# Kernel tuning notes

Measured on AMD Instinct MI355X. Metric: run time of the kernel, lower is better.

## Reference

```python
import jax, jax.numpy as jnp
import numpy as np


def setup_inputs() -> dict:
    key = jax.random.key(0)
    k1, k2, k3, k4 = jax.random.split(key, 4)
    B, Nq, Nk, D = 8, 2048, 2048, 768
    return {
        "query": jax.random.normal(k1, (B, Nq, D), dtype=jnp.float32),
        "key": jax.random.normal(k2, (Nk, D), dtype=jnp.float32),
        "x": jax.random.normal(k3, (B, Nk, D), dtype=jnp.float32),
        "W": jax.random.normal(k4, (D, D), dtype=jnp.float32) * (1.0 / np.sqrt(D)),
        "b": jnp.zeros((D,), dtype=jnp.float32),
    }


def reference(query, key, x, W, b):
    # Linear projection: [B,Nq,dk] @ W^T + b -> [B,Nq,dq]
    query_proj = jnp.einsum("bqd,ed->bqe", query, W) + b
    # tensordot over dim_query: [B,Nq,dq] x [Nk,dq] -> [B,Nq,Nk]
    score = jnp.einsum("bqe,ke->bqk", query_proj, key)
    attn = jax.nn.softmax(score, axis=-1)
    # bmm: [B,Nq,Nk] @ [B,Nk,Dv] -> [B,Nq,Dv]
    out = jnp.einsum("bqk,bkd->bqd", attn, x)
    return (out, attn)
```

## Files before the change

kernel.cpp:

```cpp
#include <hip/hip_runtime.h>

typedef short s16x8 __attribute__((ext_vector_type(8)));
typedef _Float16 h16x8 __attribute__((ext_vector_type(8)));
typedef float f32x4 __attribute__((ext_vector_type(4)));

__device__ __forceinline__ unsigned short f2bf(float f) {
    unsigned int u = __builtin_bit_cast(unsigned int, f);
    u += 0x7FFFu + ((u >> 16) & 1u);
    return (unsigned short)(u >> 16);
}
__device__ __forceinline__ float bf2f(unsigned short h) {
    unsigned int u = ((unsigned int)h) << 16;
    return __builtin_bit_cast(float, u);
}
__device__ __forceinline__ unsigned short f2h(float f) {
    _Float16 h = (_Float16)f;
    return __builtin_bit_cast(unsigned short, h);
}
__device__ __forceinline__ float h2f(unsigned short u) {
    return (float)__builtin_bit_cast(_Float16, u);
}

__device__ __forceinline__ int swz(int row, int kbyte) {
    return (row * 64 + kbyte) ^ (((row >> 1) & 3) << 4);
}

__device__ __forceinline__ void gl16(const void* g, void* l) {
    __builtin_amdgcn_global_load_lds(
        (__attribute__((address_space(1))) void*)(g),
        (__attribute__((address_space(3))) void*)(l), 16, 0, 0);
}


__global__ __launch_bounds__(256, 1) void score_2ph(
    const unsigned short* __restrict__ A, const unsigned short* __restrict__ Bm,
    const float* __restrict__ bias, float* __restrict__ C,
    int M, int N, int K, int nbx)
{
    __shared__ unsigned short lds[2][2][128 * 64];

    const int bid = blockIdx.x;
    const int cpx = gridDim.x >> 3;
    const int sw  = (bid & 7) * cpx + (bid >> 3);
    const int m0 = (sw / nbx) * 128, n0 = (sw % nbx) * 128;

    const int t = threadIdx.x;
    const int l = t & 63, w = t >> 6;
    const int rm = (w >> 1) * 64, cn = (w & 1) * 64;
    const int lr = l & 15;
    const int kg16 = (l >> 4) * 16;

    const int jrow   = l >> 3;
    const int srcoff = ((l & 7) ^ jrow) << 3;

    const unsigned short* gA = A  + (long)(m0 + jrow) * K + srcoff;
    const unsigned short* gB = Bm + (long)(n0 + jrow) * K + srcoff;

    f32x4 acc[4][4];
    #pragma unroll
    for (int i = 0; i < 4; ++i)
        #pragma unroll
        for (int j = 0; j < 4; ++j)
            acc[i][j] = (f32x4){0.f, 0.f, 0.f, 0.f};

    const int nt = K >> 6;
    #pragma unroll
    for (int i = 0; i < 4; ++i) {
        const int c = w * 4 + i;
        gl16(gA + (long)(8 * c) * K, &lds[0][0][c * 512]);
        gl16(gB + (long)(8 * c) * K, &lds[0][1][c * 512]);
    }
    __syncthreads();

    int p = 0;
    for (int it = 0; it < nt; ++it) {
        if (it + 1 < nt) {
            const unsigned short* nA = gA + (it + 1) * 64;
            const unsigned short* nB = gB + (it + 1) * 64;
            #pragma unroll
            for (int i = 0; i < 4; ++i) {
                const int c = w * 4 + i;
                gl16(nA + (long)(8 * c) * K, &lds[p ^ 1][0][c * 512]);
                gl16(nB + (long)(8 * c) * K, &lds[p ^ 1][1][c * 512]);
            }
        }
        const char* baseA = (const char*)&lds[p][0][0];
        const char* baseB = (const char*)&lds[p][1][0];
        h16x8 af[2][4], bf[2][4];
        #pragma unroll
        for (int ks = 0; ks < 2; ++ks)
            #pragma unroll
            for (int mi = 0; mi < 4; ++mi) {
                const int row = rm + mi * 16 + lr;
                af[ks][mi] = *(const h16x8*)(baseA + row * 128 +
                                ((ks * 64 + kg16) ^ ((row & 7) << 4)));
            }
        #pragma unroll
        for (int ks = 0; ks < 2; ++ks)
            #pragma unroll
            for (int nj = 0; nj < 4; ++nj) {
                const int row = cn + nj * 16 + lr;
                bf[ks][nj] = *(const h16x8*)(baseB + row * 128 +
                                ((ks * 64 + kg16) ^ ((row & 7) << 4)));
            }
        #pragma unroll
        for (int ks = 0; ks < 2; ++ks)
            #pragma unroll
            for (int mi = 0; mi < 4; ++mi)
                #pragma unroll
                for (int nj = 0; nj < 4; ++nj)
                    acc[mi][nj] = __builtin_amdgcn_mfma_f32_16x16x32_f16(
                        af[ks][mi], bf[ks][nj], acc[mi][nj], 0, 0, 0);
        __syncthreads();
        p ^= 1;
    }

    #pragma unroll
    for (int mi = 0; mi < 4; ++mi) {
        #pragma unroll
        for (int nj = 0; nj < 4; ++nj) {
            const int row = m0 + rm + mi * 16 + (l >> 4) * 4;
            const int col = n0 + cn + nj * 16 + lr;
            const float badd = bias[col];
            #pragma unroll
            for (int r = 0; r < 4; ++r)
                C[(long)(row + r) * N + col] = acc[mi][nj][r] + badd;
        }
    }
}

__global__ __launch_bounds__(256, 1) void pv_2ph(
    const unsigned short* __restrict__ A, const unsigned short* __restrict__ Bm,
    float* __restrict__ C, int M, int N, int K,
    long strideA, long strideB, long strideC)
{
    __shared__ unsigned short lds[2][2][128 * 64];

    const int bz = blockIdx.z;
    const unsigned short* Ab = A  + (long)bz * strideA;
    const unsigned short* Bb = Bm + (long)bz * strideB;
    float* Cb = C + (long)bz * strideC;
    const int m0 = blockIdx.x * 128, n0 = blockIdx.y * 128;

    const int t = threadIdx.x;
    const int l = t & 63, w = t >> 6;
    const int rm = (w >> 1) * 64, cn = (w & 1) * 64;
    const int lr = l & 15;
    const int kg16 = (l >> 4) * 16;

    const int jrow   = l >> 3;
    const int srcoff = ((l & 7) ^ jrow) << 3;

    const unsigned short* gA = Ab + (long)(m0 + jrow) * K + srcoff;
    const unsigned short* gB = Bb + (long)(n0 + jrow) * K + srcoff;

    f32x4 acc[4][4];
    #pragma unroll
    for (int i = 0; i < 4; ++i)
        #pragma unroll
        for (int j = 0; j < 4; ++j)
            acc[i][j] = (f32x4){0.f, 0.f, 0.f, 0.f};

    const int nt = K >> 6;
    #pragma unroll
    for (int i = 0; i < 4; ++i) {
        const int c = w * 4 + i;
        gl16(gA + (long)(8 * c) * K, &lds[0][0][c * 512]);
        gl16(gB + (long)(8 * c) * K, &lds[0][1][c * 512]);
    }
    __syncthreads();

    int p = 0;
    for (int it = 0; it < nt; ++it) {
        if (it + 1 < nt) {
            const unsigned short* nA = gA + (it + 1) * 64;
            const unsigned short* nB = gB + (it + 1) * 64;
            #pragma unroll
            for (int i = 0; i < 4; ++i) {
                const int c = w * 4 + i;
                gl16(nA + (long)(8 * c) * K, &lds[p ^ 1][0][c * 512]);
                gl16(nB + (long)(8 * c) * K, &lds[p ^ 1][1][c * 512]);
            }
        }
        const char* baseA = (const char*)&lds[p][0][0];
        const char* baseB = (const char*)&lds[p][1][0];
        h16x8 af[2][4], bf[2][4];
        #pragma unroll
        for (int ks = 0; ks < 2; ++ks)
            #pragma unroll
            for (int mi = 0; mi < 4; ++mi) {
                const int row = rm + mi * 16 + lr;
                af[ks][mi] = *(const h16x8*)(baseA + row * 128 +
                                ((ks * 64 + kg16) ^ ((row & 7) << 4)));
            }
        #pragma unroll
        for (int ks = 0; ks < 2; ++ks)
            #pragma unroll
            for (int nj = 0; nj < 4; ++nj) {
                const int row = cn + nj * 16 + lr;
                bf[ks][nj] = *(const h16x8*)(baseB + row * 128 +
                                ((ks * 64 + kg16) ^ ((row & 7) << 4)));
            }
        #pragma unroll
        for (int ks = 0; ks < 2; ++ks)
            #pragma unroll
            for (int mi = 0; mi < 4; ++mi)
                #pragma unroll
                for (int nj = 0; nj < 4; ++nj)
                    acc[mi][nj] = __builtin_amdgcn_mfma_f32_16x16x32_f16(
                        af[ks][mi], bf[ks][nj], acc[mi][nj], 0, 0, 0);
        __syncthreads();
        p ^= 1;
    }

    #pragma unroll
    for (int mi = 0; mi < 4; ++mi) {
        #pragma unroll
        for (int nj = 0; nj < 4; ++nj) {
            const int row = m0 + rm + mi * 16 + (l >> 4) * 4;
            const int col = n0 + cn + nj * 16 + lr;
            #pragma unroll
            for (int r = 0; r < 4; ++r)
                Cb[(long)(row + r) * N + col] = acc[mi][nj][r];
        }
    }
}

template<int SPLIT, bool TRANSB, bool BIAS>
__global__ __launch_bounds__(256, 1) void mfma_gemm(
    const float* __restrict__ A, const float* __restrict__ Bsrc,
    const float* __restrict__ bias, float* __restrict__ C,
    int M, int N, int K, long strideA, long strideB, long strideC)
{
    constexpr int NB = (SPLIT > 1) ? 2 : 1;
    __shared__ unsigned short sA[NB][128 * 32];
    __shared__ unsigned short sB[NB][128 * 32];

    const int t  = threadIdx.x;
    const int bz = blockIdx.z;
    const float* Ab = A    + (long)bz * strideA;
    const float* Bb = Bsrc + (long)bz * strideB;
    float*       Cb = C    + (long)bz * strideC;
    const int m0 = blockIdx.y * 128;
    const int n0 = blockIdx.x * 128;

    const int l  = t & 63, w = t >> 6;
    const int rm = (w >> 1) * 64;
    const int cn = (w & 1) * 64;
    const int lr = l & 15;
    const int kg = (l >> 4) * 16;

    const int srow = t >> 1;
    const int skh  = (t & 1) * 16;
    const int s_ = t & 15;
    const int kp = t >> 4;

    f32x4 acc[4][4];
    #pragma unroll
    for (int i = 0; i < 4; ++i)
        #pragma unroll
        for (int j = 0; j < 4; ++j)
            acc[i][j] = (f32x4){0.f, 0.f, 0.f, 0.f};

    for (int kt = 0; kt < K; kt += 32) {
        {
            const float* p = &Ab[(long)(m0 + srow) * K + kt + skh];
            float f[16];
            #pragma unroll
            for (int q = 0; q < 4; ++q) {
                const float4 v = *(const float4*)(p + 4 * q);
                f[4*q+0] = v.x; f[4*q+1] = v.y; f[4*q+2] = v.z; f[4*q+3] = v.w;
            }
            s16x8 h0, h1, l0, l1;
            #pragma unroll
            for (int q = 0; q < 8; ++q) {
                unsigned short h = f2bf(f[q]);      h0[q] = (short)h;
                if (SPLIT > 1) l0[q] = (short)f2bf(f[q] - bf2f(h));
                unsigned short g = f2bf(f[8 + q]);  h1[q] = (short)g;
                if (SPLIT > 1) l1[q] = (short)f2bf(f[8 + q] - bf2f(g));
            }
            *(s16x8*)((char*)sA[0] + swz(srow, skh * 2))      = h0;
            *(s16x8*)((char*)sA[0] + swz(srow, skh * 2 + 16)) = h1;
            if (SPLIT > 1) {
                *(s16x8*)((char*)sA[1] + swz(srow, skh * 2))      = l0;
                *(s16x8*)((char*)sA[1] + swz(srow, skh * 2 + 16)) = l1;
            }
        }
        if (!TRANSB) {
            const float* p = &Bb[(long)(n0 + srow) * K + kt + skh];
            float f[16];
            #pragma unroll
            for (int q = 0; q < 4; ++q) {
                const float4 v = *(const float4*)(p + 4 * q);
                f[4*q+0] = v.x; f[4*q+1] = v.y; f[4*q+2] = v.z; f[4*q+3] = v.w;
            }
            s16x8 h0, h1, l0, l1;
            #pragma unroll
            for (int q = 0; q < 8; ++q) {
                unsigned short h = f2bf(f[q]);      h0[q] = (short)h;
                if (SPLIT > 1) l0[q] = (short)f2bf(f[q] - bf2f(h));
                unsigned short g = f2bf(f[8 + q]);  h1[q] = (short)g;
                if (SPLIT > 1) l1[q] = (short)f2bf(f[8 + q] - bf2f(g));
            }
            *(s16x8*)((char*)sB[0] + swz(srow, skh * 2))      = h0;
            *(s16x8*)((char*)sB[0] + swz(srow, skh * 2 + 16)) = h1;
            if (SPLIT > 1) {
                *(s16x8*)((char*)sB[1] + swz(srow, skh * 2))      = l0;
                *(s16x8*)((char*)sB[1] + swz(srow, skh * 2 + 16)) = l1;
            }
        } else {
            const float* r0 = &Bb[(long)(kt + 2 * kp) * N + n0 + s_ * 8];
            const float* r1 = r0 + N;
            float a0[8], a1[8];
            {
                const float4 u0 = *(const float4*)(r0);
                const float4 u1 = *(const float4*)(r0 + 4);
                const float4 v0 = *(const float4*)(r1);
                const float4 v1 = *(const float4*)(r1 + 4);
                a0[0]=u0.x;a0[1]=u0.y;a0[2]=u0.z;a0[3]=u0.w;
                a0[4]=u1.x;a0[5]=u1.y;a0[6]=u1.z;a0[7]=u1.w;
                a1[0]=v0.x;a1[1]=v0.y;a1[2]=v0.z;a1[3]=v0.w;
                a1[4]=v1.x;a1[5]=v1.y;a1[6]=v1.z;a1[7]=v1.w;
            }
            #pragma unroll
            for (int j = 0; j < 8; ++j) {
                const int i  = (j + s_) & 7;
                const int nl = s_ * 8 + i;
                const unsigned int val =
                    (unsigned int)f2bf(a0[i]) | ((unsigned int)f2bf(a1[i]) << 16);
                *(unsigned int*)((char*)sB[0] + swz(nl, 4 * kp)) = val;
            }
        }
        __syncthreads();

        s16x8 ah[4], bh[4];
        #pragma unroll
        for (int mi = 0; mi < 4; ++mi)
            ah[mi] = *(const s16x8*)((const char*)sA[0] + swz(rm + mi * 16 + lr, kg));
        #pragma unroll
        for (int nj = 0; nj < 4; ++nj)
            bh[nj] = *(const s16x8*)((const char*)sB[0] + swz(cn + nj * 16 + lr, kg));
        #pragma unroll
        for (int mi = 0; mi < 4; ++mi)
            #pragma unroll
            for (int nj = 0; nj < 4; ++nj)
                acc[mi][nj] = __builtin_amdgcn_mfma_f32_16x16x32_bf16(
                    ah[mi], bh[nj], acc[mi][nj], 0, 0, 0);
        if (SPLIT > 1) {
            s16x8 al[4], bl[4];
            #pragma unroll
            for (int mi = 0; mi < 4; ++mi)
                al[mi] = *(const s16x8*)((const char*)sA[1] + swz(rm + mi * 16 + lr, kg));
            #pragma unroll
            for (int mi = 0; mi < 4; ++mi)
                #pragma unroll
                for (int nj = 0; nj < 4; ++nj)
                    acc[mi][nj] = __builtin_amdgcn_mfma_f32_16x16x32_bf16(
                        al[mi], bh[nj], acc[mi][nj], 0, 0, 0);
            #pragma unroll
            for (int nj = 0; nj < 4; ++nj)
                bl[nj] = *(const s16x8*)((const char*)sB[1] + swz(cn + nj * 16 + lr, kg));
            #pragma unroll
            for (int mi = 0; mi < 4; ++mi)
                #pragma unroll
                for (int nj = 0; nj < 4; ++nj)
                    acc[mi][nj] = __builtin_amdgcn_mfma_f32_16x16x32_bf16(
                        ah[mi], bl[nj], acc[mi][nj], 0, 0, 0);
        }
        __syncthreads();
    }

    #pragma unroll
    for (int mi = 0; mi < 4; ++mi) {
        #pragma unroll
        for (int nj = 0; nj < 4; ++nj) {
            const int row = m0 + rm + mi * 16 + (l >> 4) * 4;
            const int col = n0 + cn + nj * 16 + lr;
            const float badd = BIAS ? bias[col] : 0.f;
            #pragma unroll
            for (int r = 0; r < 4; ++r)
                Cb[(long)(row + r) * N + col] = acc[mi][nj][r] + badd;
        }
    }
}

__global__ __launch_bounds__(256, 1) void score_gemm(
    const unsigned short* __restrict__ Ah, const unsigned short* __restrict__ Al,
    const unsigned short* __restrict__ Bh, const unsigned short* __restrict__ Bl,
    const float* __restrict__ bias, float* __restrict__ C,
    int M, int N, int K, int nbx)
{
    __shared__ unsigned short sAh[128 * 32];
    __shared__ unsigned short sBh[128 * 32];
    __shared__ unsigned short sAl[128 * 32];
    __shared__ unsigned short sBl[128 * 32];

    const int bid = blockIdx.x;
    const int cpx = gridDim.x >> 3;
    const int sw  = (bid & 7) * cpx + (bid >> 3);
    const int mb  = sw / nbx, nb = sw % nbx;
    const int m0 = mb * 128, n0 = nb * 128;

    const int t = threadIdx.x;
    const int l = t & 63, w = t >> 6;
    const int rm = (w >> 1) * 64;
    const int cn = (w & 1) * 64;
    const int lr = l & 15;
    const int kg = (l >> 4) * 16;

    const int r0 = 2 * w, r1 = 2 * w + 1;
    const int rowS0 = 16 * r0 + (l >> 2);
    const int rowS1 = 16 * r1 + (l >> 2);
    const int h0 = (l & 3) ^ ((rowS0 >> 1) & 3);
    const int h1 = (l & 3) ^ ((rowS1 >> 1) & 3);

    const unsigned short* gAh0 = Ah + (long)(m0 + rowS0) * K + 8 * h0;
    const unsigned short* gAh1 = Ah + (long)(m0 + rowS1) * K + 8 * h1;
    const unsigned short* gAl0 = Al + (long)(m0 + rowS0) * K + 8 * h0;
    const unsigned short* gAl1 = Al + (long)(m0 + rowS1) * K + 8 * h1;
    const unsigned short* gBh0 = Bh + (long)(n0 + rowS0) * K + 8 * h0;
    const unsigned short* gBh1 = Bh + (long)(n0 + rowS1) * K + 8 * h1;
    const unsigned short* gBl0 = Bl + (long)(n0 + rowS0) * K + 8 * h0;
    const unsigned short* gBl1 = Bl + (long)(n0 + rowS1) * K + 8 * h1;

    unsigned short* dA0 = &sAh[r0 * 512];
    unsigned short* dA1 = &sAh[r1 * 512];
    unsigned short* dAl0 = &sAl[r0 * 512];
    unsigned short* dAl1 = &sAl[r1 * 512];
    unsigned short* dB0 = &sBh[r0 * 512];
    unsigned short* dB1 = &sBh[r1 * 512];
    unsigned short* dBl0 = &sBl[r0 * 512];
    unsigned short* dBl1 = &sBl[r1 * 512];

    f32x4 acc[4][4];
    #pragma unroll
    for (int i = 0; i < 4; ++i)
        #pragma unroll
        for (int j = 0; j < 4; ++j)
            acc[i][j] = (f32x4){0.f, 0.f, 0.f, 0.f};

    const int nk = K >> 5;
    for (int it = 0; it < nk; ++it) {
        gl16(gAh0, dA0);  gl16(gAh1, dA1);
        gl16(gBh0, dB0);  gl16(gBh1, dB1);
        gl16(gAl0, dAl0); gl16(gAl1, dAl1);
        gl16(gBl0, dBl0); gl16(gBl1, dBl1);
        gAh0 += 32; gAh1 += 32; gAl0 += 32; gAl1 += 32;
        gBh0 += 32; gBh1 += 32; gBl0 += 32; gBl1 += 32;
        __syncthreads();

        s16x8 ah[4], bh[4];
        #pragma unroll
        for (int mi = 0; mi < 4; ++mi)
            ah[mi] = *(const s16x8*)((const char*)sAh + swz(rm + mi * 16 + lr, kg));
        #pragma unroll
        for (int nj = 0; nj < 4; ++nj)
            bh[nj] = *(const s16x8*)((const char*)sBh + swz(cn + nj * 16 + lr, kg));
        #pragma unroll
        for (int mi = 0; mi < 4; ++mi)
            #pragma unroll
            for (int nj = 0; nj < 4; ++nj)
                acc[mi][nj] = __builtin_amdgcn_mfma_f32_16x16x32_bf16(
                    ah[mi], bh[nj], acc[mi][nj], 0, 0, 0);
        s16x8 al[4], bl[4];
        #pragma unroll
        for (int mi = 0; mi < 4; ++mi)
            al[mi] = *(const s16x8*)((const char*)sAl + swz(rm + mi * 16 + lr, kg));
        #pragma unroll
        for (int mi = 0; mi < 4; ++mi)
            #pragma unroll
            for (int nj = 0; nj < 4; ++nj)
                acc[mi][nj] = __builtin_amdgcn_mfma_f32_16x16x32_bf16(
                    al[mi], bh[nj], acc[mi][nj], 0, 0, 0);
        #pragma unroll
        for (int nj = 0; nj < 4; ++nj)
            bl[nj] = *(const s16x8*)((const char*)sBl + swz(cn + nj * 16 + lr, kg));
        #pragma unroll
        for (int mi = 0; mi < 4; ++mi)
            #pragma unroll
            for (int nj = 0; nj < 4; ++nj)
                acc[mi][nj] = __builtin_amdgcn_mfma_f32_16x16x32_bf16(
                    ah[mi], bl[nj], acc[mi][nj], 0, 0, 0);
        __syncthreads();
    }

    #pragma unroll
    for (int mi = 0; mi < 4; ++mi) {
        #pragma unroll
        for (int nj = 0; nj < 4; ++nj) {
            const int row = m0 + rm + mi * 16 + (l >> 4) * 4;
            const int col = n0 + cn + nj * 16 + lr;
            const float badd = bias[col];
            #pragma unroll
            for (int r = 0; r < 4; ++r)
                C[(long)(row + r) * N + col] = acc[mi][nj][r] + badd;
        }
    }
}

__global__ __launch_bounds__(256, 1) void out_gemm(
    const float* __restrict__ A32, const unsigned short* __restrict__ B16,
    float* __restrict__ C, int M, int N, int K,
    long strideA, long strideB, long strideC)
{
    __shared__ unsigned short sA[128 * 32];
    __shared__ unsigned short sB[128 * 32];

    const int bz = blockIdx.z;
    const float* Ab = A32 + (long)bz * strideA;
    const unsigned short* Bb = B16 + (long)bz * strideB;
    float* Cb = C + (long)bz * strideC;
    const int m0 = blockIdx.x * 128;
    const int n0 = blockIdx.y * 128;

    const int t = threadIdx.x;
    const int l = t & 63, w = t >> 6;
    const int rm = (w >> 1) * 64;
    const int cn = (w & 1) * 64;
    const int lr = l & 15;
    const int kg = (l >> 4) * 16;

    const int r0 = 2 * w, r1 = 2 * w + 1;
    const int rowS0 = 16 * r0 + (l >> 2);
    const int rowS1 = 16 * r1 + (l >> 2);
    const int h0 = (l & 3) ^ ((rowS0 >> 1) & 3);
    const int h1 = (l & 3) ^ ((rowS1 >> 1) & 3);
    const unsigned short* gB0 = Bb + (long)(n0 + rowS0) * K + 8 * h0;
    const unsigned short* gB1 = Bb + (long)(n0 + rowS1) * K + 8 * h1;
    unsigned short* dB0 = &sB[r0 * 512];
    unsigned short* dB1 = &sB[r1 * 512];

    const int srow = t >> 1;
    const int skh  = (t & 1) * 16;
    const float* gA = &Ab[(long)(m0 + srow) * K + skh];

    f32x4 acc[4][4];
    #pragma unroll
    for (int i = 0; i < 4; ++i)
        #pragma unroll
        for (int j = 0; j < 4; ++j)
            acc[i][j] = (f32x4){0.f, 0.f, 0.f, 0.f};

    const int nk = K >> 5;
    for (int it = 0; it < nk; ++it) {
        gl16(gB0, dB0); gl16(gB1, dB1);
        gB0 += 32; gB1 += 32;
        {
            float f[16];
            #pragma unroll
            for (int q = 0; q < 4; ++q) {
                const float4 v = *(const float4*)(gA + 4 * q);
                f[4*q+0] = v.x; f[4*q+1] = v.y; f[4*q+2] = v.z; f[4*q+3] = v.w;
            }
            gA += 32;
            s16x8 v0, v1;
            #pragma unroll
            for (int q = 0; q < 8; ++q) {
                v0[q] = (short)f2bf(f[q]);
                v1[q] = (short)f2bf(f[8 + q]);
            }
            *(s16x8*)((char*)sA + swz(srow, skh * 2))      = v0;
            *(s16x8*)((char*)sA + swz(srow, skh * 2 + 16)) = v1;
        }
        __syncthreads();

        s16x8 ah[4], bh[4];
        #pragma unroll
        for (int mi = 0; mi < 4; ++mi)
            ah[mi] = *(const s16x8*)((const char*)sA + swz(rm + mi * 16 + lr, kg));
        #pragma unroll
        for (int nj = 0; nj < 4; ++nj)
            bh[nj] = *(const s16x8*)((const char*)sB + swz(cn + nj * 16 + lr, kg));
        #pragma unroll
        for (int mi = 0; mi < 4; ++mi)
            #pragma unroll
            for (int nj = 0; nj < 4; ++nj)
                acc[mi][nj] = __builtin_amdgcn_mfma_f32_16x16x32_bf16(
                    ah[mi], bh[nj], acc[mi][nj], 0, 0, 0);
        __syncthreads();
    }

    #pragma unroll
    for (int mi = 0; mi < 4; ++mi) {
        #pragma unroll
        for (int nj = 0; nj < 4; ++nj) {
            const int row = m0 + rm + mi * 16 + (l >> 4) * 4;
            const int col = n0 + cn + nj * 16 + lr;
            #pragma unroll
            for (int r = 0; r < 4; ++r)
                Cb[(long)(row + r) * N + col] = acc[mi][nj][r];
        }
    }
}

template<int MODE>
__global__ __launch_bounds__(256) void transpose64(
    const float* __restrict__ in, void* __restrict__ outv,
    int R, int Cc, long sIn, long sOut)
{
    __shared__ float tl[64][65];
    const int z = blockIdx.z;
    const float* ib = in + (long)z * sIn;
    const int r0 = blockIdx.x * 64, c0 = blockIdx.y * 64;
    const int t = threadIdx.x;
    const int lrr = t >> 4, lc = (t & 15) * 4;
    #pragma unroll
    for (int p = 0; p < 4; ++p) {
        const float4 v = *(const float4*)&ib[(long)(r0 + lrr + 16 * p) * Cc + c0 + lc];
        tl[lrr + 16 * p][lc + 0] = v.x; tl[lrr + 16 * p][lc + 1] = v.y;
        tl[lrr + 16 * p][lc + 2] = v.z; tl[lrr + 16 * p][lc + 3] = v.w;
    }
    __syncthreads();
    #pragma unroll
    for (int p = 0; p < 4; ++p) {
        const int orow = c0 + lrr + 16 * p;
        const int ocol = r0 + lc;
        const float a = tl[lc + 0][lrr + 16 * p];
        const float b = tl[lc + 1][lrr + 16 * p];
        const float c = tl[lc + 2][lrr + 16 * p];
        const float d = tl[lc + 3][lrr + 16 * p];
        if (MODE == 1) {
            ushort4 u = { f2bf(a), f2bf(b), f2bf(c), f2bf(d) };
            *(ushort4*)((unsigned short*)outv + (long)z * sOut + (long)orow * R + ocol) = u;
        } else if (MODE == 2) {
            ushort4 u = { f2h(a), f2h(b), f2h(c), f2h(d) };
            *(ushort4*)((unsigned short*)outv + (long)z * sOut + (long)orow * R + ocol) = u;
        } else {
            float4 u = { a, b, c, d };
            *(float4*)((float*)outv + (long)z * sOut + (long)orow * R + ocol) = u;
        }
    }
}

__global__ __launch_bounds__(256) void convert_hilo(
    const float* __restrict__ src, unsigned short* __restrict__ hi,
    unsigned short* __restrict__ lo, long n8)
{
    for (long i = (long)blockIdx.x * blockDim.x + threadIdx.x; i < n8;
         i += (long)gridDim.x * blockDim.x) {
        const float4 a = *(const float4*)&src[i * 8];
        const float4 b = *(const float4*)&src[i * 8 + 4];
        const float f[8] = { a.x, a.y, a.z, a.w, b.x, b.y, b.z, b.w };
        s16x8 h, lv;
        #pragma unroll
        for (int q = 0; q < 8; ++q) {
            const unsigned short hh = f2bf(f[q]);
            h[q]  = (short)hh;
            lv[q] = (short)f2bf(f[q] - bf2f(hh));
        }
        *(s16x8*)&hi[i * 8] = h;
        *(s16x8*)&lo[i * 8] = lv;
    }
}

__global__ __launch_bounds__(256) void convert_q_ilv(
    const float* __restrict__ src, unsigned short* __restrict__ dst,
    int kd8, long n8)
{
    const int Kd = kd8 * 8;
    for (long i = (long)blockIdx.x * blockDim.x + threadIdx.x; i < n8;
         i += (long)gridDim.x * blockDim.x) {
        const long row = i / kd8;
        const int  col = (int)(i - row * kd8) * 8;
        const float4 a = *(const float4*)&src[i * 8];
        const float4 b = *(const float4*)&src[i * 8 + 4];
        const float f[8] = { a.x, a.y, a.z, a.w, b.x, b.y, b.z, b.w };
        s16x8 h, lv;
        #pragma unroll
        for (int q = 0; q < 8; ++q) {
            const unsigned short hh = f2h(f[q]);
            h[q]  = (short)hh;
            lv[q] = (short)f2h(f[q] - h2f(hh));
        }
        unsigned short* dr = dst + row * (long)(2 * Kd);
        *(s16x8*)&dr[col]      = h;
        *(s16x8*)&dr[Kd + col] = lv;
    }
}

__global__ __launch_bounds__(256) void convert_kw_dup(
    const float* __restrict__ src, unsigned short* __restrict__ dst,
    int kd8, long n8)
{
    const int Kd = kd8 * 8;
    for (long i = (long)blockIdx.x * blockDim.x + threadIdx.x; i < n8;
         i += (long)gridDim.x * blockDim.x) {
        const long row = i / kd8;
        const int  col = (int)(i - row * kd8) * 8;
        const float4 a = *(const float4*)&src[i * 8];
        const float4 b = *(const float4*)&src[i * 8 + 4];
        const float f[8] = { a.x, a.y, a.z, a.w, b.x, b.y, b.z, b.w };
        s16x8 h;
        #pragma unroll
        for (int q = 0; q < 8; ++q) h[q] = (short)f2h(f[q]);
        unsigned short* dr = dst + row * (long)(2 * Kd);
        *(s16x8*)&dr[col]      = h;
        *(s16x8*)&dr[Kd + col] = h;
    }
}

__global__ __launch_bounds__(256) void bk_dot(
    const float* __restrict__ key, const float* __restrict__ b,
    float* __restrict__ bk, int D)
{
    const int row = blockIdx.x * 4 + (threadIdx.x >> 6);
    const int l = threadIdx.x & 63;
    const float* kr = key + (long)row * D;
    float s = 0.f;
    for (int e = l; e < D; e += 64) s += kr[e] * b[e];
    #pragma unroll
    for (int off = 32; off > 0; off >>= 1) s += __shfl_xor(s, off);
    if (l == 0) bk[row] = s;
}

__global__ __launch_bounds__(256) void softmax_f16(
    float* __restrict__ S, unsigned short* __restrict__ S16, int cols)
{
    const long row = blockIdx.x;
    float* p = S + row * (long)cols;
    unsigned short* p16 = S16 + row * (long)cols;
    const int t = threadIdx.x;
    const int wid = t >> 6;
    const int base = t * 8;

    const float4 a = *(const float4*)&p[base];
    const float4 b = *(const float4*)&p[base + 4];
    float vals[8] = { a.x, a.y, a.z, a.w, b.x, b.y, b.z, b.w };
    float m = -INFINITY;
    #pragma unroll
    for (int i = 0; i < 8; ++i) m = fmaxf(m, vals[i]);
    #pragma unroll
    for (int off = 32; off > 0; off >>= 1)
        m = fmaxf(m, __shfl_xor(m, off));
    __shared__ float smax[4], ssum[4];
    if ((t & 63) == 0) smax[wid] = m;
    __syncthreads();
    m = fmaxf(fmaxf(smax[0], smax[1]), fmaxf(smax[2], smax[3]));

    float s = 0.f;
    #pragma unroll
    for (int i = 0; i < 8; ++i) {
        vals[i] = __expf(vals[i] - m);
        s += vals[i];
    }
    #pragma unroll
    for (int off = 32; off > 0; off >>= 1)
        s += __shfl_xor(s, off);
    if ((t & 63) == 0) ssum[wid] = s;
    __syncthreads();
    s = (ssum[0] + ssum[1]) + (ssum[2] + ssum[3]);
    const float inv = 1.0f / s;

    float4 o0, o1;
    o0.x = vals[0]*inv; o0.y = vals[1]*inv; o0.z = vals[2]*inv; o0.w = vals[3]*inv;
    o1.x = vals[4]*inv; o1.y = vals[5]*inv; o1.z = vals[6]*inv; o1.w = vals[7]*inv;
    *(float4*)&p[base]     = o0;
    *(float4*)&p[base + 4] = o1;
    s16x8 h;
    h[0]=(short)f2h(o0.x); h[1]=(short)f2h(o0.y); h[2]=(short)f2h(o0.z); h[3]=(short)f2h(o0.w);
    h[4]=(short)f2h(o1.x); h[5]=(short)f2h(o1.y); h[6]=(short)f2h(o1.z); h[7]=(short)f2h(o1.w);
    *(s16x8*)&p16[base] = h;
}

__global__ __launch_bounds__(256) void softmax_rows(float* __restrict__ S, int cols)
{
    const long row = blockIdx.x;
    float* p = S + row * (long)cols;
    const int t = threadIdx.x;
    const int wid = t >> 6;

    float vals[8];
    float m = -INFINITY;
    #pragma unroll
    for (int i = 0; i < 8; ++i) {
        vals[i] = p[t + i * 256];
        m = fmaxf(m, vals[i]);
    }
    #pragma unroll
    for (int off = 32; off > 0; off >>= 1)
        m = fmaxf(m, __shfl_xor(m, off));
    __shared__ float smax[4], ssum[4];
    if ((t & 63) == 0) smax[wid] = m;
    __syncthreads();
    m = fmaxf(fmaxf(smax[0], smax[1]), fmaxf(smax[2], smax[3]));

    float s = 0.f;
    #pragma unroll
    for (int i = 0; i < 8; ++i) {
        vals[i] = __expf(vals[i] - m);
        s += vals[i];
    }
    #pragma unroll
    for (int off = 32; off > 0; off >>= 1)
        s += __shfl_xor(s, off);
    if ((t & 63) == 0) ssum[wid] = s;
    __syncthreads();
    s = (ssum[0] + ssum[1]) + (ssum[2] + ssum[3]);
    const float inv = 1.0f / s;
    #pragma unroll
    for (int i = 0; i < 8; ++i)
        p[t + i * 256] = vals[i] * inv;
}

extern "C" void kernel_launch(void* const* d_in, const int* in_sizes, int n_in,
                              void* d_out, int out_size, void* d_ws, size_t ws_size,
                              hipStream_t stream)
{
    const float* query = (const float*)d_in[0];
    const float* key   = (const float*)d_in[1];
    const float* x     = (const float*)d_in[2];
    const float* W     = (const float*)d_in[3];
    const float* bias  = (const float*)d_in[4];

    const int D  = in_sizes[4];
    const int Nk = in_sizes[1] / D;
    const int B  = in_sizes[2] / (Nk * D);
    const int Nq = in_sizes[0] / (B * D);

    float* out  = (float*)d_out;
    float* attn = out + (long)B * Nq * D;

    const long nQ  = (long)B * Nq * D;
    const long nKW = (long)Nk * D;
    const long nX  = (long)B * Nk * D;
    const int  M   = B * Nq;
    const int  K2  = 2 * D;

    const size_t xTb    = (size_t)nX * 2;
    const size_t kwDupB = (size_t)Nk * K2 * 2;
    const size_t bkB    = (size_t)Nk * 4;
    const size_t atb1   = (size_t)Nq * Nk * 2;
    const size_t fixedB = xTb + kwDupB + bkB;
    const size_t qLob   = (size_t)nQ * 2;
    const size_t wsMid  = xTb + qLob;

    int g = 0;
    if (ws_size >= fixedB + 2 * atb1) {
        g = (int)((ws_size - fixedB) / atb1);
        if (g > B) g = B;
    }

    if (g >= 2) {
        unsigned short* qIlv  = (unsigned short*)out;
        unsigned short* xT     = (unsigned short*)d_ws;
        unsigned short* kwDup  = (unsigned short*)((char*)d_ws + xTb);
        float*          bk     = (float*)((char*)d_ws + xTb + kwDupB);
        unsigned short* attn16 = (unsigned short*)((char*)d_ws + fixedB);
        float* Wt  = attn;
        float* KWf = attn + 1048576;

        dim3 gtw(D / 64, D / 64, 1);
        transpose64<0><<<gtw, 256, 0, stream>>>(W, Wt, D, D, 0L, 0L);
        dim3 gkw(D / 128, Nk / 128, 1);
        mfma_gemm<3, false, false><<<gkw, 256, 0, stream>>>(
            key, Wt, nullptr, KWf, Nk, D, D, 0L, 0L, 0L);
        convert_kw_dup<<<768, 256, 0, stream>>>(KWf, kwDup, D / 8, nKW / 8);
        bk_dot<<<Nk / 4, 256, 0, stream>>>(key, bias, bk, D);
        convert_q_ilv<<<2048, 256, 0, stream>>>(query, qIlv, D / 8, nQ / 8);
        dim3 gtx(Nk / 64, D / 64, B);
        transpose64<2><<<gtx, 256, 0, stream>>>(
            x, xT, Nk, D, (long)Nk * D, (long)D * Nk);

        const int nbx = Nk / 128;
        const int nwg = (M / 128) * nbx;
        score_2ph<<<nwg, 256, 0, stream>>>(
            qIlv, kwDup, bk, attn, M, Nk, K2, nbx);

        for (int b0 = 0; b0 < B; b0 += g) {
            const int gb = (b0 + g <= B) ? g : (B - b0);
            softmax_f16<<<gb * Nq, 256, 0, stream>>>(
                attn + (long)b0 * Nq * Nk, attn16, Nk);
            dim3 go(Nq / 128, D / 128, gb);
            pv_2ph<<<go, 256, 0, stream>>>(
                attn16, xT + (long)b0 * D * Nk, out + (long)b0 * Nq * D,
                Nq, D, Nk, (long)Nq * Nk, (long)D * Nk, (long)Nq * D);
        }
    } else if (ws_size >= wsMid) {
        unsigned short* q_hi  = (unsigned short*)out;
        unsigned short* KW_hi = q_hi + nQ;
        unsigned short* KW_lo = KW_hi + nKW;
        float*          bk    = (float*)(KW_lo + nKW);
        unsigned short* q_lo  = (unsigned short*)d_ws;
        unsigned short* xT    = q_lo + nQ;
        float* Wt  = attn;
        float* KWf = attn + 1048576;

        dim3 gtw(D / 64, D / 64, 1);
        transpose64<0><<<gtw, 256, 0, stream>>>(W, Wt, D, D, 0L, 0L);
        dim3 gkw(D / 128, Nk / 128, 1);
        mfma_gemm<3, false, false><<<gkw, 256, 0, stream>>>(
            key, Wt, nullptr, KWf, Nk, D, D, 0L, 0L, 0L);
        convert_hilo<<<768, 256, 0, stream>>>(KWf, KW_hi, KW_lo, nKW / 8);
        bk_dot<<<Nk / 4, 256, 0, stream>>>(key, bias, bk, D);
        convert_hilo<<<2048, 256, 0, stream>>>(query, q_hi, q_lo, nQ / 8);
        dim3 gtx(Nk / 64, D / 64, B);
        transpose64<1><<<gtx, 256, 0, stream>>>(
            x, xT, Nk, D, (long)Nk * D, (long)D * Nk);
        const int nbx = Nk / 128;
        const int nwg = (B * Nq / 128) * nbx;
        score_gemm<<<nwg, 256, 0, stream>>>(
            q_hi, q_lo, KW_hi, KW_lo, bk, attn, B * Nq, Nk, D, nbx);
        softmax_rows<<<B * Nq, 256, 0, stream>>>(attn, Nk);
        dim3 go(Nq / 128, D / 128, B);
        out_gemm<<<go, 256, 0, stream>>>(
            attn, xT, out, Nq, D, Nk, (long)Nq * Nk, (long)D * Nk, (long)Nq * D);
    } else {
        float* qp = out;
        dim3 g1(D / 128, (B * Nq) / 128, 1);
        mfma_gemm<3, false, true><<<g1, 256, 0, stream>>>(
            query, W, bias, qp, B * Nq, D, D, 0L, 0L, 0L);
        dim3 g2(Nk / 128, Nq / 128, B);
        mfma_gemm<3, false, false><<<g2, 256, 0, stream>>>(
            qp, key, nullptr, attn, Nq, Nk, D, (long)Nq * D, 0L, (long)Nq * Nk);
        softmax_rows<<<B * Nq, 256, 0, stream>>>(attn, Nk);
        dim3 g4(D / 128, Nq / 128, B);
        mfma_gemm<1, true, false><<<g4, 256, 0, stream>>>(
            attn, x, nullptr, out, Nq, D, Nk, (long)Nq * Nk, (long)Nk * D, (long)Nq * D);
    }
}
```

Baseline: 347.9 us.

## Replace score GEMM with 256x256 tile, 8-wave, four-phase pipelined kernel

The score GEMM moves from a 128x128 tile with 4 waves and simple double buffering to a 256x256 tile with 8 waves. Each K-step is split into four sub-phases, with global-to-LDS loads for upcoming tiles interleaved between them using explicit vmcnt waits, barriers and raised priority around the MFMA bursts. The aim is more data reuse per tile and better overlap of memory traffic with MFMA compute. In exchange the block count drops fourfold, which may hurt occupancy and tail balance across CUs. The hand-tuned wait counts are also fragile.

```diff
diff --git a/kernel.cpp b/kernel.cpp
--- a/kernel.cpp
+++ b/kernel.cpp
@@ -31,102 +31,133 @@
         (__attribute__((address_space(3))) void*)(l), 16, 0, 0);
 }
 
-
-__global__ __launch_bounds__(256, 1) void score_2ph(
+#define STG(ptr, rowbase, tau, bufp, slot) do {                                     \
+    gl16((ptr) + (long)((rowbase) + sl) * K + (tau) * 64 + koff,                    \
+         &lds[bufp][slot][(unsigned)t * 8]);                                        \
+    gl16((ptr) + (long)((rowbase) + 64 + sl) * K + (tau) * 64 + koff,               \
+         &lds[bufp][slot][4096u + (unsigned)t * 8]);                                \
+} while (0)
+
+#define PH(bufp, qi, qj, VMSTR, STAGEBLOCK) do {                                    \
+    h16x8 af_[2][4], bf_[2][2];                                                     \
+    const char* baseA_ = (const char*)&lds[bufp][qi][0];                            \
+    const char* baseB_ = (const char*)&lds[bufp][2 + (qj)][0];                      \
+    _Pragma("unroll")                                                               \
+    for (int ks_ = 0; ks_ < 2; ++ks_) {                                             \
+        _Pragma("unroll")                                                           \
+        for (int f_ = 0; f_ < 4; ++f_) {                                            \
+            const int row_ = wm * 64 + f_ * 16 + lr;                                \
+            af_[ks_][f_] = *(const h16x8*)(baseA_ + row_ * 128 +                    \
+                            ((ks_ * 64 + kg16) ^ ((row_ & 7) << 4)));               \
+        }                                                                           \
+        _Pragma("unroll")                                                           \
+        for (int g_ = 0; g_ < 2; ++g_) {                                            \
+            const int row_ = wn * 32 + g_ * 16 + lr;                                \
+            bf_[ks_][g_] = *(const h16x8*)(baseB_ + row_ * 128 +                    \
+                            ((ks_ * 64 + kg16) ^ ((row_ & 7) << 4)));               \
+        }                                                                           \
+    }                                                                               \
+    STAGEBLOCK;                                                                     \
+    asm volatile("s_waitcnt vmcnt(" VMSTR ")" ::: "memory");                        \
+    __builtin_amdgcn_s_barrier();                                                   \
+    __builtin_amdgcn_sched_barrier(0);                                              \
+    __builtin_amdgcn_s_setprio(1);                                                  \
+    _Pragma("unroll")                                                               \
+    for (int ks_ = 0; ks_ < 2; ++ks_)                                               \
+        _Pragma("unroll")                                                           \
+        for (int f_ = 0; f_ < 4; ++f_)                                              \
+            _Pragma("unroll")                                                       \
+            for (int g_ = 0; g_ < 2; ++g_)                                          \
+                acc[qi][qj][f_][g_] = __builtin_amdgcn_mfma_f32_16x16x32_f16(       \
+                    af_[ks_][f_], bf_[ks_][g_], acc[qi][qj][f_][g_], 0, 0, 0);      \
+    __builtin_amdgcn_s_setprio(0);                                                  \
+    __builtin_amdgcn_s_barrier();                                                   \
+    __builtin_amdgcn_sched_barrier(0);                                              \
+} while (0)
+
+__global__ __launch_bounds__(512, 2) void score_8ph(
     const unsigned short* __restrict__ A, const unsigned short* __restrict__ Bm,
     const float* __restrict__ bias, float* __restrict__ C,
     int M, int N, int K, int nbx)
 {
-    __shared__ unsigned short lds[2][2][128 * 64];
+    __shared__ unsigned short lds[2][4][8192];
 
     const int bid = blockIdx.x;
     const int cpx = gridDim.x >> 3;
     const int sw  = (bid & 7) * cpx + (bid >> 3);
-    const int m0 = (sw / nbx) * 128, n0 = (sw % nbx) * 128;
+    const int m0 = (sw / nbx) * 256, n0 = (sw % nbx) * 256;
 
     const int t = threadIdx.x;
     const int l = t & 63, w = t >> 6;
-    const int rm = (w >> 1) * 64, cn = (w & 1) * 64;
+    const int wm = w >> 2, wn = w & 3;
     const int lr = l & 15;
     const int kg16 = (l >> 4) * 16;
 
-    const int jrow   = l >> 3;
-    const int srcoff = ((l & 7) ^ jrow) << 3;
-
-    const unsigned short* gA = A  + (long)(m0 + jrow) * K + srcoff;
-    const unsigned short* gB = Bm + (long)(n0 + jrow) * K + srcoff;
-
-    f32x4 acc[4][4];
-    #pragma unroll
-    for (int i = 0; i < 4; ++i)
-        #pragma unroll
-        for (int j = 0; j < 4; ++j)
-            acc[i][j] = (f32x4){0.f, 0.f, 0.f, 0.f};
+    const int sl   = w * 8 + (l >> 3);
+    const int koff = ((l & 7) ^ (sl & 7)) * 8;
+
+    f32x4 acc[2][2][4][2];
+    #pragma unroll
+    for (int a = 0; a < 2; ++a)
+        #pragma unroll
+        for (int b = 0; b < 2; ++b)
+            #pragma unroll
+            for (int c = 0; c < 4; ++c)
+                #pragma unroll
+                for (int d = 0; d < 2; ++d)
+                    acc[a][b][c][d] = (f32x4){0.f, 0.f, 0.f, 0.f};
 
     const int nt = K >> 6;
-    #pragma unroll
-    for (int i = 0; i < 4; ++i) {
-        const int c = w * 4 + i;
-        gl16(gA + (long)(8 * c) * K, &lds[0][0][c * 512]);
-        gl16(gB + (long)(8 * c) * K, &lds[0][1][c * 512]);
-    }
-    __syncthreads();
-
-    int p = 0;
-    for (int it = 0; it < nt; ++it) {
-        if (it + 1 < nt) {
-            const unsigned short* nA = gA + (it + 1) * 64;
-            const unsigned short* nB = gB + (it + 1) * 64;
-            #pragma unroll
-            for (int i = 0; i < 4; ++i) {
-                const int c = w * 4 + i;
-                gl16(nA + (long)(8 * c) * K, &lds[p ^ 1][0][c * 512]);
-                gl16(nB + (long)(8 * c) * K, &lds[p ^ 1][1][c * 512]);
-            }
-        }
-        const char* baseA = (const char*)&lds[p][0][0];
-        const char* baseB = (const char*)&lds[p][1][0];
-        h16x8 af[2][4], bf[2][4];
-        #pragma unroll
-        for (int ks = 0; ks < 2; ++ks)
-            #pragma unroll
-            for (int mi = 0; mi < 4; ++mi) {
-                const int row = rm + mi * 16 + lr;
-                af[ks][mi] = *(const h16x8*)(baseA + row * 128 +
-                                ((ks * 64 + kg16) ^ ((row & 7) << 4)));
-            }
-        #pragma unroll
-        for (int ks = 0; ks < 2; ++ks)
-            #pragma unroll
-            for (int nj = 0; nj < 4; ++nj) {
-                const int row = cn + nj * 16 + lr;
-                bf[ks][nj] = *(const h16x8*)(baseB + row * 128 +
-                                ((ks * 64 + kg16) ^ ((row & 7) << 4)));
-            }
-        #pragma unroll
-        for (int ks = 0; ks < 2; ++ks)
-            #pragma unroll
-            for (int mi = 0; mi < 4; ++mi)
+
+    STG(A,  m0,       0, 0, 0);
+    STG(Bm, n0,       0, 0, 2);
+    STG(A,  m0 + 128, 0, 0, 1);
+    STG(Bm, n0 + 128, 0, 0, 3);
+    STG(A,  m0,       1, 1, 0);
+    STG(Bm, n0,       1, 1, 2);
+    asm volatile("s_waitcnt vmcnt(8)" ::: "memory");
+    __builtin_amdgcn_s_barrier();
+    __builtin_amdgcn_sched_barrier(0);
+
+    int tau = 0;
+    for (; tau < nt - 2; ++tau) {
+        const int bp = tau & 1;
+        PH(bp, 0, 0, "6",  { STG(A,  m0 + 128, tau + 1, bp ^ 1, 1); });
+        PH(bp, 0, 1, "10", { STG(Bm, n0 + 128, tau + 1, bp ^ 1, 3); });
+        PH(bp, 1, 0, "10", { STG(A,  m0,       tau + 2, bp,     0); });
+        PH(bp, 1, 1, "8",  { STG(Bm, n0,       tau + 2, bp,     2); });
+    }
+    {
+        const int bp = tau & 1;
+        PH(bp, 0, 0, "6",  { STG(A,  m0 + 128, tau + 1, bp ^ 1, 1); });
+        PH(bp, 0, 1, "10", { STG(Bm, n0 + 128, tau + 1, bp ^ 1, 3); });
+        PH(bp, 1, 0, "10", {});
+        PH(bp, 1, 1, "8",  {});
+        ++tau;
+    }
+    {
+        const int bp = tau & 1;
+        PH(bp, 0, 0, "0", {});
+        PH(bp, 0, 1, "0", {});
+        PH(bp, 1, 0, "0", {});
+        PH(bp, 1, 1, "0", {});
+    }
+
+    #pragma unroll
+    for (int qi = 0; qi < 2; ++qi)
+        #pragma unroll
+        for (int qj = 0; qj < 2; ++qj)
+            #pragma unroll
+            for (int f = 0; f < 4; ++f)
                 #pragma unroll
-                for (int nj = 0; nj < 4; ++nj)
-                    acc[mi][nj] = __builtin_amdgcn_mfma_f32_16x16x32_f16(
-                        af[ks][mi], bf[ks][nj], acc[mi][nj], 0, 0, 0);
-        __syncthreads();
-        p ^= 1;
-    }
-
-    #pragma unroll
-    for (int mi = 0; mi < 4; ++mi) {
-        #pragma unroll
-        for (int nj = 0; nj < 4; ++nj) {
-            const int row = m0 + rm + mi * 16 + (l >> 4) * 4;
-            const int col = n0 + cn + nj * 16 + lr;
-            const float badd = bias[col];
-            #pragma unroll
-            for (int r = 0; r < 4; ++r)
-                C[(long)(row + r) * N + col] = acc[mi][nj][r] + badd;
-        }
-    }
+                for (int g = 0; g < 2; ++g) {
+                    const int row = m0 + qi * 128 + wm * 64 + f * 16 + (l >> 4) * 4;
+                    const int col = n0 + qj * 128 + wn * 32 + g * 16 + lr;
+                    const float badd = bias[col];
+                    #pragma unroll
+                    for (int r = 0; r < 4; ++r)
+                        C[(long)(row + r) * N + col] = acc[qi][qj][f][g][r] + badd;
+                }
 }
 
 __global__ __launch_bounds__(256, 1) void pv_2ph(
@@ -861,9 +892,9 @@
         transpose64<2><<<gtx, 256, 0, stream>>>(
             x, xT, Nk, D, (long)Nk * D, (long)D * Nk);
 
-        const int nbx = Nk / 128;
-        const int nwg = (M / 128) * nbx;
-        score_2ph<<<nwg, 256, 0, stream>>>(
+        const int nbx = Nk / 256;
+        const int nwg = (M / 256) * nbx;
+        score_8ph<<<nwg, 512, 0, stream>>>(
             qIlv, kwDup, bk, attn, M, Nk, K2, nbx);
 
         for (int b0 = 0; b0 < B; b0 += g) {
```

New measurement: 348.8 us. About the same (+0.2%).
